# Performance work log

Hardware: AMD Instinct MI355X
Metric: run time of the kernel (lower is better)

## Reference

```python
import math
import jax, jax.numpy as jnp
import numpy as np

B, T, D, V, L, H = 2, 1024, 768, 32768, 4, 12
HD = D // H
STD = 0.02


def layer_norm(x, w, b):
    mu = x.mean(-1, keepdims=True)
    var = ((x - mu) ** 2).mean(-1, keepdims=True)
    return (x - mu) * jax.lax.rsqrt(var + 1e-5) * w + b


def new_gelu(x):
    c = math.sqrt(2.0 / math.pi)
    return 0.5 * x * (1.0 + jnp.tanh(c * (x + 0.044715 * x ** 3)))


def setup_inputs() -> dict:
    key = jax.random.key(0)
    ks = jax.random.split(key, 10)
    idx = jax.random.randint(ks[0], (B, T), 0, V)
    age = jax.random.uniform(ks[1], (B, T), dtype=jnp.float32) * 36500.0  # days
    wte = jax.random.normal(ks[2], (V, D), jnp.float32) * STD  # tied with lm_head
    wae_w = jax.random.normal(ks[3], (D, D), jnp.float32) * STD  # AgeEncoding linear (no bias)
    proj_std = STD / math.sqrt(2 * L)
    return {
        'idx': idx,
        'age': age,
        'wte': wte,
        'wae_w': wae_w,
        'ln1_w': jnp.ones((L, D), jnp.float32),
        'ln1_b': jnp.zeros((L, D), jnp.float32),
        'attn_w': jax.random.normal(ks[4], (L, 3 * D, D), jnp.float32) * STD,
        'attn_b': jnp.zeros((L, 3 * D), jnp.float32),
        'proj_w': jax.random.normal(ks[5], (L, D, D), jnp.float32) * proj_std,
        'proj_b': jnp.zeros((L, D), jnp.float32),
        'ln2_w': jnp.ones((L, D), jnp.float32),
        'ln2_b': jnp.zeros((L, D), jnp.float32),
        'fc_w': jax.random.normal(ks[6], (L, 4 * D, D), jnp.float32) * STD,
        'fc_b': jnp.zeros((L, 4 * D), jnp.float32),
        'fc2_w': jax.random.normal(ks[7], (L, D, 4 * D), jnp.float32) * proj_std,
        'fc2_b': jnp.zeros((L, D), jnp.float32),
        'lnf_w': jnp.ones((D,), jnp.float32),
        'lnf_b': jnp.zeros((D,), jnp.float32),
    }


def _forward(idx, age, wte, wae_w, ln1_w, ln1_b, attn_w, attn_b, proj_w, proj_b,
             ln2_w, ln2_b, fc_w, fc_b, fc2_w, fc2_b, lnf_w, lnf_b):
    # token embedding (tied with lm_head)
    tok = wte[idx]  # [B,T,D]
    # age encoding: interleaved sin/cos of age/365.25 * div_term, then linear
    div = jnp.exp(jnp.arange(0, D, 2).astype(jnp.float32) * (-math.log(10000.0) / D))  # [D/2]
    ang = (age[..., None] / 365.25) * div  # [B,T,D/2]
    y = jnp.zeros((B, T, D), tok.dtype)
    y = y.at[..., 0::2].set(jnp.sin(ang)).at[..., 1::2].set(jnp.cos(ang))
    x = tok + y @ wae_w.T  # token_drop identity at dropout 0 (scaled by 1-0)

    # attention mask: valid-token outer product, causal, plus self-attn for pad tokens
    valid = idx > 0
    tril = jnp.tril(jnp.ones((T, T), bool))
    mask = valid[:, None, None, :] & valid[:, None, :, None] & tril
    mask = (mask | ((~valid)[:, None, None, :] & jnp.eye(T, dtype=bool))) & tril  # [B,1,T,T]

    scale = 1.0 / math.sqrt(HD)

    def block(x, p):
        l1w, l1b, aw, ab, pw, pb, l2w, l2b, fw, fb, f2w, f2b = p
        h = layer_norm(x, l1w, l1b)
        qkv = h @ aw.T + ab
        q, k, v = jnp.split(qkv, 3, axis=-1)
        q = q.reshape(B, T, H, HD).transpose(0, 2, 1, 3)  # [B,H,T,HD]
        k = k.reshape(B, T, H, HD).transpose(0, 2, 1, 3)
        v = v.reshape(B, T, H, HD).transpose(0, 2, 1, 3)
        att = jnp.einsum('bhqd,bhkd->bhqk', q, k) * scale
        att = jnp.where(mask, att, -jnp.inf)
        att = jax.nn.softmax(att, axis=-1)
        yv = jnp.einsum('bhqk,bhkd->bhqd', att, v)
        yv = yv.transpose(0, 2, 1, 3).reshape(B, T, D)
        x = x + yv @ pw.T + pb
        h2 = layer_norm(x, l2w, l2b)
        x = x + new_gelu(h2 @ fw.T + fb) @ f2w.T + f2b
        return x, att

    x, att = jax.lax.scan(block, x, (ln1_w, ln1_b, attn_w, attn_b, proj_w, proj_b,
                                     ln2_w, ln2_b, fc_w, fc_b, fc2_w, fc2_b))
    x = layer_norm(x, lnf_w, lnf_b)
    logits = x @ wte.T  # tied lm_head
    return logits


def reference(idx, age, wte, wae_w, ln1_w, ln1_b, attn_w, attn_b, proj_w, proj_b,
              ln2_w, ln2_b, fc_w, fc_b, fc2_w, fc2_b, lnf_w, lnf_b):
    return _forward(idx, age, wte, wae_w, ln1_w, ln1_b, attn_w, attn_b, proj_w, proj_b,
                    ln2_w, ln2_b, fc_w, fc_b, fc2_w, fc2_b, lnf_w, lnf_b)
```

## Files before the change

### kernel.cpp

```cpp
#include <hip/hip_runtime.h>

typedef unsigned short u16;
typedef __bf16 bf16x8 __attribute__((ext_vector_type(8)));
typedef float f32x4 __attribute__((ext_vector_type(4)));

__device__ __forceinline__ u16 f2bf(float f) {
    union { float f; unsigned int u; } c; c.f = f;
    unsigned int u = c.u;
    unsigned int r = (u + 0x7FFFu + ((u >> 16) & 1u)) >> 16;
    return (u16)r;
}

__device__ __forceinline__ float gelu_f(float v) {
    const float c = 0.7978845608028654f;
    float t = tanhf(c * (v + 0.044715f * v * v * v));
    return 0.5f * v * (1.0f + t);
}

typedef const __attribute__((address_space(1))) unsigned int* as1_u32p;
typedef __attribute__((address_space(3))) unsigned int* as3_u32p;
__device__ __forceinline__ void gload16(const void* g, void* l) {
    __builtin_amdgcn_global_load_lds((as1_u32p)g, (as3_u32p)l, 16, 0, 0);
}

__global__ __launch_bounds__(256) void cvt_kernel(
    const float* __restrict__ src, u16* __restrict__ dst, int n4)
{
    int i = blockIdx.x * 256 + threadIdx.x;
    int stride = gridDim.x * 256;
    for (; i < n4; i += stride) {
        float4 f = reinterpret_cast<const float4*>(src)[i];
        union { u16 h[4]; uint2 u; } cv;
        cv.h[0] = f2bf(f.x); cv.h[1] = f2bf(f.y);
        cv.h[2] = f2bf(f.z); cv.h[3] = f2bf(f.w);
        reinterpret_cast<uint2*>(dst)[i] = cv.u;
    }
}

__global__ __launch_bounds__(256) void embed_kernel(
    const int* __restrict__ idx, const float* __restrict__ age,
    const float* __restrict__ wte, float* __restrict__ x, u16* __restrict__ y)
{
    int t = blockIdx.x;
    int tid = threadIdx.x;
    int tok = idx[t];
    float a = age[t] * (1.0f / 365.25f);
    const float kc = -9.210340371976184f / 768.0f;
#pragma unroll
    for (int j = 0; j < 3; j++) {
        int d = tid + j * 256;
        x[(size_t)t * 768 + d] = wte[(size_t)tok * 768 + d];
        int twoi = d & ~1;
        float dv = __expf(kc * (float)twoi);
        float ang = a * dv;
        float val = (d & 1) ? __cosf(ang) : __sinf(ang);
        y[(size_t)t * 768 + d] = f2bf(val);
    }
}

__global__ __launch_bounds__(256) void ln_kernel(
    const float* __restrict__ x, const float* __restrict__ w,
    const float* __restrict__ b, u16* __restrict__ out)
{
    int row = blockIdx.x;
    int tid = threadIdx.x;
    int l = tid & 63, wv = tid >> 6;
    const float* xr = x + (size_t)row * 768;
    float v[3], s = 0.f, ss = 0.f;
#pragma unroll
    for (int j = 0; j < 3; j++) { v[j] = xr[tid + j * 256]; s += v[j]; ss += v[j] * v[j]; }
#pragma unroll
    for (int d = 1; d < 64; d <<= 1) { s += __shfl_xor(s, d); ss += __shfl_xor(ss, d); }
    __shared__ float ps[4], pss[4];
    if (l == 0) { ps[wv] = s; pss[wv] = ss; }
    __syncthreads();
    s = ps[0] + ps[1] + ps[2] + ps[3];
    ss = pss[0] + pss[1] + pss[2] + pss[3];
    float mu = s * (1.0f / 768.0f);
    float var = ss * (1.0f / 768.0f) - mu * mu;
    float rstd = rsqrtf(var + 1e-5f);
#pragma unroll
    for (int j = 0; j < 3; j++) {
        int d = tid + j * 256;
        out[(size_t)row * 768 + d] = f2bf((v[j] - mu) * rstd * w[d] + b[d]);
    }
}

enum { EPI_BF16 = 0, EPI_BF16_GELU = 1, EPI_F32_RESID = 2, EPI_F32 = 3 };

template <int EPI>
__global__ __launch_bounds__(256) void gemm_lds_kernel(
    const u16* __restrict__ A, const u16* __restrict__ B,
    const float* __restrict__ bias, const float* resid, void* out,
    int N, int K, int mtiles, int nwg8)
{
    __shared__ u16 As[128][32];
    __shared__ u16 Bs[128][32];
    int tid = threadIdx.x;
    int l = tid & 63, w = tid >> 6;
    int lw = l & 15, lg = l >> 4;
    int bid = blockIdx.x;
    int wg = (bid & 7) * nwg8 + (bid >> 3);
    int mt = wg % mtiles, nt = wg / mtiles;
    int row0 = mt * 128, col0 = nt * 128;
    int mbase = (w & 1) * 64, nbase = (w >> 1) * 64;

    int srow = w * 32 + (l >> 2);
    int scol = (l & 3) * 8;
    const u16* ga = A + (size_t)(row0 + srow) * K + scol;
    const u16* gb = B + (size_t)(col0 + srow) * K + scol;
    u16* lA0 = &As[w * 32][0];
    u16* lA1 = &As[w * 32 + 16][0];
    u16* lB0 = &Bs[w * 32][0];
    u16* lB1 = &Bs[w * 32 + 16][0];
    const size_t k16 = (size_t)16 * K;

    f32x4 acc[4][4] = {};
    for (int kk = 0; kk < K; kk += 32) {
        gload16(ga + kk, lA0);
        gload16(ga + k16 + kk, lA1);
        gload16(gb + kk, lB0);
        gload16(gb + k16 + kk, lB1);
        __syncthreads();
        bf16x8 af[4], bfr[4];
#pragma unroll
        for (int mi = 0; mi < 4; mi++)
            af[mi] = *reinterpret_cast<const bf16x8*>(&As[mbase + mi * 16 + lw][lg * 8]);
#pragma unroll
        for (int ni = 0; ni < 4; ni++)
            bfr[ni] = *reinterpret_cast<const bf16x8*>(&Bs[nbase + ni * 16 + lw][lg * 8]);
#pragma unroll
        for (int mi = 0; mi < 4; mi++)
#pragma unroll
            for (int ni = 0; ni < 4; ni++)
                acc[mi][ni] = __builtin_amdgcn_mfma_f32_16x16x32_bf16(af[mi], bfr[ni], acc[mi][ni], 0, 0, 0);
        __syncthreads();
    }

#pragma unroll
    for (int mi = 0; mi < 4; mi++) {
#pragma unroll
        for (int ni = 0; ni < 4; ni++) {
            int colc = col0 + nbase + ni * 16 + lw;
            float bv = bias ? bias[colc] : 0.0f;
#pragma unroll
            for (int j = 0; j < 4; j++) {
                int row = row0 + mbase + mi * 16 + lg * 4 + j;
                size_t off = (size_t)row * N + colc;
                float v = acc[mi][ni][j] + bv;
                if constexpr (EPI == EPI_BF16) {
                    ((u16*)out)[off] = f2bf(v);
                } else if constexpr (EPI == EPI_BF16_GELU) {
                    ((u16*)out)[off] = f2bf(gelu_f(v));
                } else if constexpr (EPI == EPI_F32_RESID) {
                    ((float*)out)[off] = v + resid[off];
                } else {
                    ((float*)out)[off] = v;
                }
            }
        }
    }
}

template <int EPI>
__global__ __launch_bounds__(256) void gemm_kernel(
    const u16* __restrict__ A, const float* __restrict__ Bw,
    const float* __restrict__ bias, const float* resid, void* out,
    int N, int K)
{
    constexpr int M = 2048;
    __shared__ u16 As[128][40];
    __shared__ u16 Bs[128][40];
    int tid = threadIdx.x;
    int l = tid & 63, w = tid >> 6;
    int lw = l & 15, lg = l >> 4;
    int mtiles = M / 128;
    int mt = blockIdx.x % mtiles, nt = blockIdx.x / mtiles;
    int row0 = mt * 128, col0 = nt * 128;
    int mbase = (w & 1) * 64, nbase = (w >> 1) * 64;
    f32x4 acc[4][4] = {};

    for (int kk = 0; kk < K; kk += 32) {
        int c = tid;
#pragma unroll
        for (int i = 0; i < 2; i++, c += 256) {
            int r = c >> 2, q = c & 3;
            uint4 u = *reinterpret_cast<const uint4*>(A + (size_t)(row0 + r) * K + kk + q * 8);
            *reinterpret_cast<uint4*>(&As[r][q * 8]) = u;
        }
        int c2 = tid;
#pragma unroll
        for (int i = 0; i < 4; i++, c2 += 256) {
            int r = c2 >> 3, q = c2 & 7;
            const float4 f = *reinterpret_cast<const float4*>(Bw + (size_t)(col0 + r) * K + kk + q * 4);
            union { u16 h[4]; uint2 u; } cv;
            cv.h[0] = f2bf(f.x); cv.h[1] = f2bf(f.y); cv.h[2] = f2bf(f.z); cv.h[3] = f2bf(f.w);
            *reinterpret_cast<uint2*>(&Bs[r][q * 4]) = cv.u;
        }
        __syncthreads();
        bf16x8 af[4], bfr[4];
#pragma unroll
        for (int mi = 0; mi < 4; mi++)
            af[mi] = *reinterpret_cast<const bf16x8*>(&As[mbase + mi * 16 + lw][lg * 8]);
#pragma unroll
        for (int ni = 0; ni < 4; ni++)
            bfr[ni] = *reinterpret_cast<const bf16x8*>(&Bs[nbase + ni * 16 + lw][lg * 8]);
#pragma unroll
        for (int mi = 0; mi < 4; mi++)
#pragma unroll
            for (int ni = 0; ni < 4; ni++)
                acc[mi][ni] = __builtin_amdgcn_mfma_f32_16x16x32_bf16(af[mi], bfr[ni], acc[mi][ni], 0, 0, 0);
        __syncthreads();
    }

#pragma unroll
    for (int mi = 0; mi < 4; mi++) {
#pragma unroll
        for (int ni = 0; ni < 4; ni++) {
            int colc = col0 + nbase + ni * 16 + lw;
            float bv = bias ? bias[colc] : 0.0f;
#pragma unroll
            for (int j = 0; j < 4; j++) {
                int row = row0 + mbase + mi * 16 + lg * 4 + j;
                size_t off = (size_t)row * N + colc;
                float v = acc[mi][ni][j] + bv;
                if constexpr (EPI == EPI_BF16) {
                    ((u16*)out)[off] = f2bf(v);
                } else if constexpr (EPI == EPI_BF16_GELU) {
                    ((u16*)out)[off] = f2bf(gelu_f(v));
                } else if constexpr (EPI == EPI_F32_RESID) {
                    ((float*)out)[off] = v + resid[off];
                } else {
                    ((float*)out)[off] = v;
                }
            }
        }
    }
}

__global__ __launch_bounds__(256) void attn_kernel(
    const u16* __restrict__ qkv, const int* __restrict__ idx, u16* __restrict__ yv)
{
    __shared__ u16 Kt[32][72];
    __shared__ u16 Vt[64][40];
    __shared__ u16 Pb[4][16][40];
    __shared__ int kval[32];

    int tid = threadIdx.x, l = tid & 63, w = tid >> 6;
    int lw = l & 15, lg = l >> 4;
    int bid = blockIdx.x;
    int qb = bid & 15;
    int h = (bid >> 4) % 12;
    int b = bid / (16 * 12);
    const size_t base = (size_t)b * 1024;

    int qrow = qb * 64 + w * 16 + lw;
    const u16* qp = qkv + (base + qrow) * 2304 + h * 64;
    bf16x8 aq0 = *reinterpret_cast<const bf16x8*>(qp + lg * 8);
    bf16x8 aq1 = *reinterpret_cast<const bf16x8*>(qp + 32 + lg * 8);

    int rowj[4], vq[4];
#pragma unroll
    for (int j = 0; j < 4; j++) {
        rowj[j] = qb * 64 + w * 16 + lg * 4 + j;
        vq[j] = idx[base + rowj[j]] > 0;
    }
    float m[4], lsum[4];
    f32x4 O[4] = {};
#pragma unroll
    for (int j = 0; j < 4; j++) { m[j] = -__builtin_inff(); lsum[j] = 0.0f; }

    int kvend = qb * 64 + 64;
    for (int kv0 = 0; kv0 < kvend; kv0 += 32) {
        {
            int r = tid >> 3, cc = tid & 7;
            const u16* kp = qkv + (base + kv0 + r) * 2304 + 768 + h * 64 + cc * 8;
            uint4 ku = *reinterpret_cast<const uint4*>(kp);
            *reinterpret_cast<uint4*>(&Kt[r][cc * 8]) = ku;
            const u16* vp = qkv + (base + kv0 + r) * 2304 + 1536 + h * 64 + cc * 8;
            union { uint4 u; u16 h8[8]; } vu;
            vu.u = *reinterpret_cast<const uint4*>(vp);
#pragma unroll
            for (int j2 = 0; j2 < 8; j2++) Vt[cc * 8 + j2][r] = vu.h8[j2];
            if (tid < 32) kval[tid] = idx[base + kv0 + tid] > 0;
        }
        __syncthreads();

        f32x4 S[2];
#pragma unroll
        for (int g = 0; g < 2; g++) {
            bf16x8 bk0 = *reinterpret_cast<const bf16x8*>(&Kt[g * 16 + lw][lg * 8]);
            bf16x8 bk1 = *reinterpret_cast<const bf16x8*>(&Kt[g * 16 + lw][32 + lg * 8]);
            f32x4 t = {};
            t = __builtin_amdgcn_mfma_f32_16x16x32_bf16(aq0, bk0, t, 0, 0, 0);
            t = __builtin_amdgcn_mfma_f32_16x16x32_bf16(aq1, bk1, t, 0, 0, 0);
            S[g] = t;
        }
        float p[2][4];
#pragma unroll
        for (int j = 0; j < 4; j++) {
            float sv0, sv1;
#pragma unroll
            for (int g = 0; g < 2; g++) {
                int kcol = kv0 + g * 16 + lw;
                float s = S[g][j] * 0.125f;
                bool keep = (kcol <= rowj[j]) &&
                            ((vq[j] && kval[g * 16 + lw]) || (kcol == rowj[j]));
                s = keep ? s : -__builtin_inff();
                if (g) sv1 = s; else sv0 = s;
            }
            float mx = fmaxf(sv0, sv1);
            mx = fmaxf(mx, __shfl_xor(mx, 1));
            mx = fmaxf(mx, __shfl_xor(mx, 2));
            mx = fmaxf(mx, __shfl_xor(mx, 4));
            mx = fmaxf(mx, __shfl_xor(mx, 8));
            float mn = fmaxf(m[j], mx);
            float mclamp = fmaxf(mn, -1e30f);
            float scale = __expf(m[j] - mclamp);
            float p0 = __expf(sv0 - mclamp);
            float p1 = __expf(sv1 - mclamp);
            float rs = p0 + p1;
            rs += __shfl_xor(rs, 1); rs += __shfl_xor(rs, 2);
            rs += __shfl_xor(rs, 4); rs += __shfl_xor(rs, 8);
            lsum[j] = lsum[j] * scale + rs;
            m[j] = mn;
#pragma unroll
            for (int ni = 0; ni < 4; ni++) O[ni][j] *= scale;
            p[0][j] = p0; p[1][j] = p1;
        }
#pragma unroll
        for (int g = 0; g < 2; g++)
#pragma unroll
            for (int j = 0; j < 4; j++)
                Pb[w][lg * 4 + j][g * 16 + lw] = f2bf(p[g][j]);
        bf16x8 ap = *reinterpret_cast<const bf16x8*>(&Pb[w][lw][lg * 8]);
#pragma unroll
        for (int ni = 0; ni < 4; ni++) {
            bf16x8 bv = *reinterpret_cast<const bf16x8*>(&Vt[ni * 16 + lw][lg * 8]);
            O[ni] = __builtin_amdgcn_mfma_f32_16x16x32_bf16(ap, bv, O[ni], 0, 0, 0);
        }
        __syncthreads();
    }

#pragma unroll
    for (int j = 0; j < 4; j++) {
        float inv = 1.0f / lsum[j];
#pragma unroll
        for (int ni = 0; ni < 4; ni++) {
            float v = O[ni][j] * inv;
            yv[(base + rowj[j]) * 768 + h * 64 + ni * 16 + lw] = f2bf(v);
        }
    }
}

static void launch_gemm_lds(int epi, const u16* A, const u16* B, const float* bias,
                            const float* resid, void* out, int N, int K, hipStream_t s)
{
    int mtiles = 2048 / 128;
    int nwg = mtiles * (N / 128);
    dim3 grid(nwg), blk(256);
    int nwg8 = nwg / 8;
    switch (epi) {
        case EPI_BF16:      gemm_lds_kernel<EPI_BF16><<<grid, blk, 0, s>>>(A, B, bias, resid, out, N, K, mtiles, nwg8); break;
        case EPI_BF16_GELU: gemm_lds_kernel<EPI_BF16_GELU><<<grid, blk, 0, s>>>(A, B, bias, resid, out, N, K, mtiles, nwg8); break;
        case EPI_F32_RESID: gemm_lds_kernel<EPI_F32_RESID><<<grid, blk, 0, s>>>(A, B, bias, resid, out, N, K, mtiles, nwg8); break;
        default:            gemm_lds_kernel<EPI_F32><<<grid, blk, 0, s>>>(A, B, bias, resid, out, N, K, mtiles, nwg8); break;
    }
}

static void launch_gemm_f32w(int epi, const u16* A, const float* Bw, const float* bias,
                             const float* resid, void* out, int N, int K, hipStream_t s)
{
    dim3 grid((2048 / 128) * (N / 128)), blk(256);
    switch (epi) {
        case EPI_BF16:      gemm_kernel<EPI_BF16><<<grid, blk, 0, s>>>(A, Bw, bias, resid, out, N, K); break;
        case EPI_BF16_GELU: gemm_kernel<EPI_BF16_GELU><<<grid, blk, 0, s>>>(A, Bw, bias, resid, out, N, K); break;
        case EPI_F32_RESID: gemm_kernel<EPI_F32_RESID><<<grid, blk, 0, s>>>(A, Bw, bias, resid, out, N, K); break;
        default:            gemm_kernel<EPI_F32><<<grid, blk, 0, s>>>(A, Bw, bias, resid, out, N, K); break;
    }
}

static void cvt(const float* src, u16* dst, size_t n, hipStream_t s) {
    int n4 = (int)(n / 4);
    int blocks = (n4 + 255) / 256;
    if (blocks > 2048) blocks = 2048;
    cvt_kernel<<<blocks, 256, 0, s>>>(src, dst, n4);
}

extern "C" void kernel_launch(void* const* d_in, const int* in_sizes, int n_in,
                              void* d_out, int out_size, void* d_ws, size_t ws_size,
                              hipStream_t stream)
{
    (void)in_sizes; (void)n_in; (void)out_size;
    const int*   idx    = (const int*)  d_in[0];
    const float* age    = (const float*)d_in[1];
    const float* wte    = (const float*)d_in[2];
    const float* wae_w  = (const float*)d_in[3];
    const float* ln1_w  = (const float*)d_in[4];
    const float* ln1_b  = (const float*)d_in[5];
    const float* attn_w = (const float*)d_in[6];
    const float* attn_b = (const float*)d_in[7];
    const float* proj_w = (const float*)d_in[8];
    const float* proj_b = (const float*)d_in[9];
    const float* ln2_w  = (const float*)d_in[10];
    const float* ln2_b  = (const float*)d_in[11];
    const float* fc_w   = (const float*)d_in[12];
    const float* fc_b   = (const float*)d_in[13];
    const float* fc2_w  = (const float*)d_in[14];
    const float* fc2_b  = (const float*)d_in[15];
    const float* lnf_w  = (const float*)d_in[16];
    const float* lnf_b  = (const float*)d_in[17];

    char* ws = (char*)d_ws;
    size_t off = 0;
    float* x   = (float*)(ws + off); off += (size_t)2048 * 768 * 4;
    u16* hb    = (u16*)(ws + off);   off += (size_t)2048 * 768 * 2;
    u16* qkvb  = (u16*)(ws + off);   off += (size_t)2048 * 2304 * 2;
    u16* yvb   = (u16*)(ws + off);   off += (size_t)2048 * 768 * 2;
    u16* a1b   = (u16*)(ws + off);   off += (size_t)2048 * 3072 * 2;
    u16* yage  = (u16*)(ws + off);   off += (size_t)2048 * 768 * 2;
    u16* wte_b  = (u16*)(ws + off);  off += (size_t)32768 * 768 * 2;
    u16* attn_wb= (u16*)(ws + off);  off += (size_t)4 * 2304 * 768 * 2;
    u16* proj_wb= (u16*)(ws + off);  off += (size_t)4 * 768 * 768 * 2;
    u16* fc_wb  = (u16*)(ws + off);  off += (size_t)4 * 3072 * 768 * 2;
    u16* fc2_wb = (u16*)(ws + off);  off += (size_t)4 * 768 * 3072 * 2;
    u16* wae_wb = (u16*)(ws + off);  off += (size_t)768 * 768 * 2;
    const size_t NEED = off;

    if (ws_size >= NEED) {
        cvt(wte,    wte_b,   (size_t)32768 * 768, stream);
        cvt(attn_w, attn_wb, (size_t)4 * 2304 * 768, stream);
        cvt(proj_w, proj_wb, (size_t)4 * 768 * 768, stream);
        cvt(fc_w,   fc_wb,   (size_t)4 * 3072 * 768, stream);
        cvt(fc2_w,  fc2_wb,  (size_t)4 * 768 * 3072, stream);
        cvt(wae_w,  wae_wb,  (size_t)768 * 768, stream);

        embed_kernel<<<2048, 256, 0, stream>>>(idx, age, wte, x, yage);
        launch_gemm_lds(EPI_F32_RESID, yage, wae_wb, nullptr, x, x, 768, 768, stream);

        for (int li = 0; li < 4; li++) {
            ln_kernel<<<2048, 256, 0, stream>>>(x, ln1_w + li * 768, ln1_b + li * 768, hb);
            launch_gemm_lds(EPI_BF16, hb, attn_wb + (size_t)li * 2304 * 768, attn_b + li * 2304,
                            nullptr, qkvb, 2304, 768, stream);
            attn_kernel<<<2 * 12 * 16, 256, 0, stream>>>(qkvb, idx, yvb);
            launch_gemm_lds(EPI_F32_RESID, yvb, proj_wb + (size_t)li * 768 * 768, proj_b + li * 768,
                            x, x, 768, 768, stream);
            ln_kernel<<<2048, 256, 0, stream>>>(x, ln2_w + li * 768, ln2_b + li * 768, hb);
            launch_gemm_lds(EPI_BF16_GELU, hb, fc_wb + (size_t)li * 3072 * 768, fc_b + li * 3072,
                            nullptr, a1b, 3072, 768, stream);
            launch_gemm_lds(EPI_F32_RESID, a1b, fc2_wb + (size_t)li * 768 * 3072, fc2_b + li * 768,
                            x, x, 768, 3072, stream);
        }

        ln_kernel<<<2048, 256, 0, stream>>>(x, lnf_w, lnf_b, hb);
        launch_gemm_lds(EPI_F32, hb, wte_b, nullptr, nullptr, d_out, 32768, 768, stream);
    } else {
        embed_kernel<<<2048, 256, 0, stream>>>(idx, age, wte, x, yage);
        launch_gemm_f32w(EPI_F32_RESID, yage, wae_w, nullptr, x, x, 768, 768, stream);
        for (int li = 0; li < 4; li++) {
            ln_kernel<<<2048, 256, 0, stream>>>(x, ln1_w + li * 768, ln1_b + li * 768, hb);
            launch_gemm_f32w(EPI_BF16, hb, attn_w + (size_t)li * 2304 * 768, attn_b + li * 2304,
                             nullptr, qkvb, 2304, 768, stream);
            attn_kernel<<<2 * 12 * 16, 256, 0, stream>>>(qkvb, idx, yvb);
            launch_gemm_f32w(EPI_F32_RESID, yvb, proj_w + (size_t)li * 768 * 768, proj_b + li * 768,
                             x, x, 768, 768, stream);
            ln_kernel<<<2048, 256, 0, stream>>>(x, ln2_w + li * 768, ln2_b + li * 768, hb);
            launch_gemm_f32w(EPI_BF16_GELU, hb, fc_w + (size_t)li * 3072 * 768, fc_b + li * 3072,
                             nullptr, a1b, 3072, 768, stream);
            launch_gemm_f32w(EPI_F32_RESID, a1b, fc2_w + (size_t)li * 768 * 3072, fc2_b + li * 768,
                             x, x, 768, 3072, stream);
        }
        ln_kernel<<<2048, 256, 0, stream>>>(x, lnf_w, lnf_b, hb);
        launch_gemm_f32w(EPI_F32, hb, wte, nullptr, nullptr, d_out, 32768, 768, stream);
    }
}
```

Measured before the change: 1.758 ms.

## Double-buffer GEMM LDS tiles and use 64-row tiles for N=768

Replaces the single-buffered LDS GEMM with a double-buffered version that prefetches the next K tile into the alternate buffer while MFMAs run on the current one, dropping one barrier per iteration. It also raises wave priority around the MFMA block. For N=768 GEMMs it uses 64x128 tiles with all four waves split along N, doubling the workgroup count so more CUs stay busy. The cost is twice the LDS use and fewer accumulators per wave on the small-tile path.

```diff
diff --git a/kernel.cpp b/kernel.cpp
--- a/kernel.cpp
+++ b/kernel.cpp
@@ -88,59 +88,74 @@
 
 enum { EPI_BF16 = 0, EPI_BF16_GELU = 1, EPI_F32_RESID = 2, EPI_F32 = 3 };
 
-template <int EPI>
-__global__ __launch_bounds__(256) void gemm_lds_kernel(
+template <int EPI, int BM, int NWM>
+__global__ __launch_bounds__(256) void gemm_db_kernel(
     const u16* __restrict__ A, const u16* __restrict__ B,
     const float* __restrict__ bias, const float* resid, void* out,
     int N, int K, int mtiles, int nwg8)
 {
-    __shared__ u16 As[128][32];
-    __shared__ u16 Bs[128][32];
+    constexpr int NWN = 4 / NWM;
+    constexpr int MI  = (BM / NWM) / 16;
+    constexpr int NI  = (128 / NWN) / 16;
+    constexpr int ASHOTS = (BM * 4) / 256;
+    __shared__ u16 As[2][BM][32];
+    __shared__ u16 Bs[2][128][32];
     int tid = threadIdx.x;
     int l = tid & 63, w = tid >> 6;
     int lw = l & 15, lg = l >> 4;
     int bid = blockIdx.x;
     int wg = (bid & 7) * nwg8 + (bid >> 3);
     int mt = wg % mtiles, nt = wg / mtiles;
-    int row0 = mt * 128, col0 = nt * 128;
-    int mbase = (w & 1) * 64, nbase = (w >> 1) * 64;
-
-    int srow = w * 32 + (l >> 2);
-    int scol = (l & 3) * 8;
-    const u16* ga = A + (size_t)(row0 + srow) * K + scol;
-    const u16* gb = B + (size_t)(col0 + srow) * K + scol;
-    u16* lA0 = &As[w * 32][0];
-    u16* lA1 = &As[w * 32 + 16][0];
-    u16* lB0 = &Bs[w * 32][0];
-    u16* lB1 = &Bs[w * 32 + 16][0];
-    const size_t k16 = (size_t)16 * K;
-
-    f32x4 acc[4][4] = {};
-    for (int kk = 0; kk < K; kk += 32) {
-        gload16(ga + kk, lA0);
-        gload16(ga + k16 + kk, lA1);
-        gload16(gb + kk, lB0);
-        gload16(gb + k16 + kk, lB1);
+    int row0 = mt * BM, col0 = nt * 128;
+    int wm = w % NWM, wn = w / NWM;
+    int mbase = wm * (BM / NWM), nbase = wn * (128 / NWN);
+
+    f32x4 acc[MI][NI] = {};
+    const int ntiles = K >> 5;
+
+    auto stage = [&](int nb, int kk) {
+        u16* asb = &As[nb][0][0];
+        u16* bsb = &Bs[nb][0][0];
+#pragma unroll
+        for (int s = 0; s < ASHOTS; s++) {
+            int c = s * 256 + tid;
+            int r = c >> 2, q = (c & 3) * 8;
+            gload16(A + (size_t)(row0 + r) * K + kk + q, asb + r * 32 + q);
+        }
+#pragma unroll
+        for (int s = 0; s < 2; s++) {
+            int c = s * 256 + tid;
+            int r = c >> 2, q = (c & 3) * 8;
+            gload16(B + (size_t)(col0 + r) * K + kk + q, bsb + r * 32 + q);
+        }
+    };
+
+    stage(0, 0);
+    __syncthreads();
+    for (int t = 0; t < ntiles; ++t) {
+        int cur = t & 1;
+        if (t + 1 < ntiles) stage(cur ^ 1, (t + 1) << 5);
+        bf16x8 af[MI], bfr[NI];
+#pragma unroll
+        for (int mi = 0; mi < MI; mi++)
+            af[mi] = *reinterpret_cast<const bf16x8*>(&As[cur][mbase + mi * 16 + lw][lg * 8]);
+#pragma unroll
+        for (int ni = 0; ni < NI; ni++)
+            bfr[ni] = *reinterpret_cast<const bf16x8*>(&Bs[cur][nbase + ni * 16 + lw][lg * 8]);
+        __builtin_amdgcn_s_setprio(1);
+#pragma unroll
+        for (int mi = 0; mi < MI; mi++)
+#pragma unroll
+            for (int ni = 0; ni < NI; ni++)
+                acc[mi][ni] = __builtin_amdgcn_mfma_f32_16x16x32_bf16(af[mi], bfr[ni], acc[mi][ni], 0, 0, 0);
+        __builtin_amdgcn_s_setprio(0);
         __syncthreads();
-        bf16x8 af[4], bfr[4];
-#pragma unroll
-        for (int mi = 0; mi < 4; mi++)
-            af[mi] = *reinterpret_cast<const bf16x8*>(&As[mbase + mi * 16 + lw][lg * 8]);
-#pragma unroll
-        for (int ni = 0; ni < 4; ni++)
-            bfr[ni] = *reinterpret_cast<const bf16x8*>(&Bs[nbase + ni * 16 + lw][lg * 8]);
-#pragma unroll
-        for (int mi = 0; mi < 4; mi++)
-#pragma unroll
-            for (int ni = 0; ni < 4; ni++)
-                acc[mi][ni] = __builtin_amdgcn_mfma_f32_16x16x32_bf16(af[mi], bfr[ni], acc[mi][ni], 0, 0, 0);
-        __syncthreads();
-    }
-
-#pragma unroll
-    for (int mi = 0; mi < 4; mi++) {
-#pragma unroll
-        for (int ni = 0; ni < 4; ni++) {
+    }
+
+#pragma unroll
+    for (int mi = 0; mi < MI; mi++) {
+#pragma unroll
+        for (int ni = 0; ni < NI; ni++) {
             int colc = col0 + nbase + ni * 16 + lw;
             float bv = bias ? bias[colc] : 0.0f;
 #pragma unroll
@@ -353,18 +368,34 @@
     }
 }
 
-static void launch_gemm_lds(int epi, const u16* A, const u16* B, const float* bias,
-                            const float* resid, void* out, int N, int K, hipStream_t s)
-{
-    int mtiles = 2048 / 128;
-    int nwg = mtiles * (N / 128);
-    dim3 grid(nwg), blk(256);
-    int nwg8 = nwg / 8;
-    switch (epi) {
-        case EPI_BF16:      gemm_lds_kernel<EPI_BF16><<<grid, blk, 0, s>>>(A, B, bias, resid, out, N, K, mtiles, nwg8); break;
-        case EPI_BF16_GELU: gemm_lds_kernel<EPI_BF16_GELU><<<grid, blk, 0, s>>>(A, B, bias, resid, out, N, K, mtiles, nwg8); break;
-        case EPI_F32_RESID: gemm_lds_kernel<EPI_F32_RESID><<<grid, blk, 0, s>>>(A, B, bias, resid, out, N, K, mtiles, nwg8); break;
-        default:            gemm_lds_kernel<EPI_F32><<<grid, blk, 0, s>>>(A, B, bias, resid, out, N, K, mtiles, nwg8); break;
+static void launch_gemm_db(int epi, const u16* A, const u16* B, const float* bias,
+                           const float* resid, void* out, int N, int K, hipStream_t s)
+{
+    dim3 blk(256);
+    if (N == 768) {
+        constexpr int BM = 64, NWM = 1;
+        int mtiles = 2048 / BM;
+        int nwg = mtiles * (N / 128);
+        dim3 grid(nwg);
+        int nwg8 = nwg / 8;
+        switch (epi) {
+            case EPI_BF16:      gemm_db_kernel<EPI_BF16, BM, NWM><<<grid, blk, 0, s>>>(A, B, bias, resid, out, N, K, mtiles, nwg8); break;
+            case EPI_BF16_GELU: gemm_db_kernel<EPI_BF16_GELU, BM, NWM><<<grid, blk, 0, s>>>(A, B, bias, resid, out, N, K, mtiles, nwg8); break;
+            case EPI_F32_RESID: gemm_db_kernel<EPI_F32_RESID, BM, NWM><<<grid, blk, 0, s>>>(A, B, bias, resid, out, N, K, mtiles, nwg8); break;
+            default:            gemm_db_kernel<EPI_F32, BM, NWM><<<grid, blk, 0, s>>>(A, B, bias, resid, out, N, K, mtiles, nwg8); break;
+        }
+    } else {
+        constexpr int BM = 128, NWM = 2;
+        int mtiles = 2048 / BM;
+        int nwg = mtiles * (N / 128);
+        dim3 grid(nwg);
+        int nwg8 = nwg / 8;
+        switch (epi) {
+            case EPI_BF16:      gemm_db_kernel<EPI_BF16, BM, NWM><<<grid, blk, 0, s>>>(A, B, bias, resid, out, N, K, mtiles, nwg8); break;
+            case EPI_BF16_GELU: gemm_db_kernel<EPI_BF16_GELU, BM, NWM><<<grid, blk, 0, s>>>(A, B, bias, resid, out, N, K, mtiles, nwg8); break;
+            case EPI_F32_RESID: gemm_db_kernel<EPI_F32_RESID, BM, NWM><<<grid, blk, 0, s>>>(A, B, bias, resid, out, N, K, mtiles, nwg8); break;
+            default:            gemm_db_kernel<EPI_F32, BM, NWM><<<grid, blk, 0, s>>>(A, B, bias, resid, out, N, K, mtiles, nwg8); break;
+        }
     }
 }
 
@@ -436,24 +467,24 @@
         cvt(wae_w,  wae_wb,  (size_t)768 * 768, stream);
 
         embed_kernel<<<2048, 256, 0, stream>>>(idx, age, wte, x, yage);
-        launch_gemm_lds(EPI_F32_RESID, yage, wae_wb, nullptr, x, x, 768, 768, stream);
+        launch_gemm_db(EPI_F32_RESID, yage, wae_wb, nullptr, x, x, 768, 768, stream);
 
         for (int li = 0; li < 4; li++) {
             ln_kernel<<<2048, 256, 0, stream>>>(x, ln1_w + li * 768, ln1_b + li * 768, hb);
-            launch_gemm_lds(EPI_BF16, hb, attn_wb + (size_t)li * 2304 * 768, attn_b + li * 2304,
-                            nullptr, qkvb, 2304, 768, stream);
+            launch_gemm_db(EPI_BF16, hb, attn_wb + (size_t)li * 2304 * 768, attn_b + li * 2304,
+                           nullptr, qkvb, 2304, 768, stream);
             attn_kernel<<<2 * 12 * 16, 256, 0, stream>>>(qkvb, idx, yvb);
-            launch_gemm_lds(EPI_F32_RESID, yvb, proj_wb + (size_t)li * 768 * 768, proj_b + li * 768,
-                            x, x, 768, 768, stream);
+            launch_gemm_db(EPI_F32_RESID, yvb, proj_wb + (size_t)li * 768 * 768, proj_b + li * 768,
+                           x, x, 768, 768, stream);
             ln_kernel<<<2048, 256, 0, stream>>>(x, ln2_w + li * 768, ln2_b + li * 768, hb);
-            launch_gemm_lds(EPI_BF16_GELU, hb, fc_wb + (size_t)li * 3072 * 768, fc_b + li * 3072,
-                            nullptr, a1b, 3072, 768, stream);
-            launch_gemm_lds(EPI_F32_RESID, a1b, fc2_wb + (size_t)li * 768 * 3072, fc2_b + li * 768,
-                            x, x, 768, 3072, stream);
+            launch_gemm_db(EPI_BF16_GELU, hb, fc_wb + (size_t)li * 3072 * 768, fc_b + li * 3072,
+                           nullptr, a1b, 3072, 768, stream);
+            launch_gemm_db(EPI_F32_RESID, a1b, fc2_wb + (size_t)li * 768 * 3072, fc2_b + li * 768,
+                           x, x, 768, 3072, stream);
         }
 
         ln_kernel<<<2048, 256, 0, stream>>>(x, lnf_w, lnf_b, hb);
-        launch_gemm_lds(EPI_F32, hb, wte_b, nullptr, nullptr, d_out, 32768, 768, stream);
+        launch_gemm_db(EPI_F32, hb, wte_b, nullptr, nullptr, d_out, 32768, 768, stream);
     } else {
         embed_kernel<<<2048, 256, 0, stream>>>(idx, age, wte, x, yage);
         launch_gemm_f32w(EPI_F32_RESID, yage, wae_w, nullptr, x, x, 768, 768, stream);
```

After: 1.553 ms. 11.6% less time.
